# Performance work log

Measured on AMD Instinct MI355X. Metric: run time of the kernel, lower is better.

## Reference

```python
import jax, jax.numpy as jnp
import numpy as np

PAD = 0  # padding_index
BIG = 10000.0

B, S = 1024, 128
V, E, H, T = 200, 512, 512, 24


def setup_inputs() -> dict:
    key = jax.random.key(0)
    ks = jax.random.split(key, 12)
    sequences = jax.random.randint(ks[0], (B, S), 0, V, dtype=jnp.int32)
    labels = jax.random.randint(ks[1], (B, S), 0, T, dtype=jnp.int32)
    true_lengths = jax.random.randint(ks[2], (B,), 1, S, dtype=jnp.int32)
    emb = jax.random.normal(ks[3], (V, E), dtype=jnp.float32) * 0.1
    emb = emb.at[PAD].set(0.0)  # nn.Embedding padding_idx zeros that row
    w1 = jax.random.normal(ks[4], (H, H), dtype=jnp.float32) * (1.0 / np.sqrt(H))
    b1 = jax.random.normal(ks[5], (H,), dtype=jnp.float32) * 0.01
    w2 = jax.random.normal(ks[6], (T, H), dtype=jnp.float32) * (1.0 / np.sqrt(H))
    b2 = jax.random.normal(ks[7], (T,), dtype=jnp.float32) * 0.01
    start_trans = jax.random.uniform(ks[8], (T,), jnp.float32, -0.1, 0.1)
    end_trans = jax.random.uniform(ks[9], (T,), jnp.float32, -0.1, 0.1)
    transitions = jax.random.uniform(ks[10], (T, T), jnp.float32, -0.1, 0.1)
    return {"sequences": sequences, "labels": labels, "true_lengths": true_lengths,
            "emb": emb, "w1": w1, "b1": b1, "w2": w2, "b2": b2,
            "start_trans": start_trans, "end_trans": end_trans, "transitions": transitions}


def _emissions(sequences, emb, w1, b1, w2, b2):
    pad_mask = (sequences == PAD).astype(jnp.float32)  # [B,S]
    x = emb[sequences]                                  # [B,S,E]
    h = jax.nn.relu(x @ w1.T + b1)                      # [B,S,H]
    scores = jax.nn.relu(h @ w2.T + b2)                 # [B,S,T]
    scores = scores.at[:, :, PAD].add(pad_mask * BIG)
    return scores


def _crf_nll_mean(emissions, labels, start_trans, end_trans, transitions):
    # emissions [B,S,T], labels [B,S]; mask = all ones (none passed in forward)
    # numerator: score of gold path
    em_gold = jnp.take_along_axis(emissions, labels[..., None], axis=2)[..., 0]  # [B,S]
    num = (start_trans[labels[:, 0]]
           + em_gold.sum(axis=1)
           + transitions[labels[:, :-1], labels[:, 1:]].sum(axis=1)
           + end_trans[labels[:, -1]])  # [B]
    # denominator: forward algorithm via scan over time
    em_t = jnp.swapaxes(emissions, 0, 1)  # [S,B,T]
    alpha0 = start_trans[None, :] + em_t[0]  # [B,T]

    def step(alpha, emit):
        # alpha [B,T_prev], transitions [T_prev,T_next], emit [B,T_next]
        nxt = jax.nn.logsumexp(alpha[:, :, None] + transitions[None] + emit[:, None, :], axis=1)
        return nxt, None

    alpha, _ = jax.lax.scan(step, alpha0, em_t[1:])
    denom = jax.nn.logsumexp(alpha + end_trans[None, :], axis=1)  # [B]
    llh = num - denom
    return -jnp.mean(llh)


def reference(sequences, labels, true_lengths, emb, w1, b1, w2, b2,
              start_trans, end_trans, transitions):
    emissions = _emissions(sequences, emb, w1, b1, w2, b2)
    return _crf_nll_mean(emissions, labels, start_trans, end_trans, transitions)
```

## Files before the change

### kernel.cpp

```cpp
#include <hip/hip_runtime.h>
#include <math.h>

#define PAD_IDX 0
#define BIGV 10000.0f
constexpr int B_ = 1024, S_ = 128, V_ = 200, E_ = 512, H_ = 512, T_ = 24;

constexpr int OFF_H  = 262144;
constexpr int OFF_EM = 364544;
constexpr int OFF_W  = 369344;
constexpr int OFF_MX = 374144;
constexpr int OFF_GP = 374344;

typedef __attribute__((ext_vector_type(8)))  short    bf8frag;
typedef __attribute__((ext_vector_type(16))) float    facc16;
typedef __attribute__((ext_vector_type(4)))  unsigned u32x4;

__device__ __forceinline__ unsigned short f2bf(float f) {
    unsigned u = __float_as_uint(f);
    u += 0x7fffu + ((u >> 16) & 1u);
    return (unsigned short)(u >> 16);
}
__device__ __forceinline__ unsigned pkbf(float lo, float hi) {
    const unsigned a = __float_as_uint(lo), b = __float_as_uint(hi);
    return ((a + 0x8000u) >> 16) | ((b + 0x8000u) & 0xffff0000u);
}

__global__ __launch_bounds__(256) void transpose_kernel(
    const float* __restrict__ w1, unsigned short* __restrict__ w1Tb,
    float* __restrict__ out)
{
    __shared__ float tile[64][65];
    const int bi = blockIdx.x >> 3, bj = blockIdx.x & 7;
    const int tx = threadIdx.x & 63, r0 = (threadIdx.x >> 6) * 16;
    if (blockIdx.x == 0 && threadIdx.x == 0) out[0] = 0.f;
    #pragma unroll
    for (int m = 0; m < 16; ++m) {
        const int r = r0 + m;
        tile[r][tx] = w1[(size_t)(bi * 64 + r) * 512 + bj * 64 + tx];
    }
    __syncthreads();
    #pragma unroll
    for (int m = 0; m < 16; ++m) {
        const int r = r0 + m;
        w1Tb[(size_t)(bj * 64 + r) * 512 + bi * 64 + tx] = f2bf(tile[tx][r]);
    }
}

__global__ __launch_bounds__(256) void h_kernel(
    const float* __restrict__ emb, const unsigned short* __restrict__ w1Tb,
    const float* __restrict__ b1, float* __restrict__ h_ws)
{
    __shared__ float xi[2 * E_];
    __shared__ float part_s[4][64][8];
    const int pair = blockIdx.x >> 1, half = blockIdx.x & 1;
    const int v0 = pair * 2, v1 = v0 + 1;
    const int tid = threadIdx.x;
    {
        const float* __restrict__ x0 = emb + (size_t)v0 * E_;
        const float* __restrict__ x1 = emb + (size_t)v1 * E_;
        #pragma unroll
        for (int m = 0; m < 2; ++m) {
            const int k = tid + m * 256;
            xi[2 * k]     = x0[k];
            xi[2 * k + 1] = x1[k];
        }
    }
    __syncthreads();
    const int part = tid >> 6, quad = tid & 63;
    const int t0 = half * 256 + quad * 4, k0 = part * 128;
    float a0 = 0.f, a1 = 0.f, a2 = 0.f, a3 = 0.f;
    float c0 = 0.f, c1 = 0.f, c2 = 0.f, c3 = 0.f;
    const unsigned short* __restrict__ wp = w1Tb + (size_t)k0 * H_ + t0;
    const float2* __restrict__ xp = (const float2*)xi + k0;
    #pragma unroll 4
    for (int i = 0; i < 128; ++i) {
        const uint2 wu = *(const uint2*)(wp + (size_t)i * H_);
        const float2 x = xp[i];
        const float w0 = __uint_as_float(wu.x << 16);
        const float w1v = __uint_as_float(wu.x & 0xffff0000u);
        const float w2v = __uint_as_float(wu.y << 16);
        const float w3v = __uint_as_float(wu.y & 0xffff0000u);
        a0 = fmaf(w0,  x.x, a0); a1 = fmaf(w1v, x.x, a1);
        a2 = fmaf(w2v, x.x, a2); a3 = fmaf(w3v, x.x, a3);
        c0 = fmaf(w0,  x.y, c0); c1 = fmaf(w1v, x.y, c1);
        c2 = fmaf(w2v, x.y, c2); c3 = fmaf(w3v, x.y, c3);
    }
    part_s[part][quad][0] = a0; part_s[part][quad][1] = a1;
    part_s[part][quad][2] = a2; part_s[part][quad][3] = a3;
    part_s[part][quad][4] = c0; part_s[part][quad][5] = c1;
    part_s[part][quad][6] = c2; part_s[part][quad][7] = c3;
    __syncthreads();
    {
        const int q2 = tid >> 2, r0 = tid & 3;
        const float s0 = (part_s[0][q2][r0]     + part_s[1][q2][r0])
                       + (part_s[2][q2][r0]     + part_s[3][q2][r0]);
        const float s1 = (part_s[0][q2][r0 + 4] + part_s[1][q2][r0 + 4])
                       + (part_s[2][q2][r0 + 4] + part_s[3][q2][r0 + 4]);
        const int t = half * 256 + tid;
        const float bb = b1[t];
        h_ws[(size_t)v0 * H_ + t] = fmaxf(s0 + bb, 0.f);
        h_ws[(size_t)v1 * H_ + t] = fmaxf(s1 + bb, 0.f);
    }
}

__global__ __launch_bounds__(256) void emis_kernel(
    const float* __restrict__ h_ws, const float* __restrict__ w2,
    const float* __restrict__ b2, float* __restrict__ em_table,
    float* __restrict__ w_table, float* __restrict__ emax_arr)
{
    __shared__ float em_row[32];
    const int v = blockIdx.x;
    const int t = threadIdx.x;
    const int wave = t >> 6, lane = t & 63;
    const float* __restrict__ hrow = h_ws + (size_t)v * H_;
    for (int jj2 = 0; jj2 < 6; ++jj2) {
        const int jo = wave * 6 + jj2;
        float part = 0.f;
        #pragma unroll
        for (int m = 0; m < H_ / 64; ++m) {
            const int k = lane + m * 64;
            part = fmaf(hrow[k], w2[(size_t)jo * H_ + k], part);
        }
        #pragma unroll
        for (int off = 32; off; off >>= 1)
            part += __shfl_xor(part, off, 64);
        if (lane == 0) {
            float val = fmaxf(part + b2[jo], 0.f);
            if (v == 0 && jo == PAD_IDX) val += BIGV;
            em_row[jo] = val;
        }
    }
    __syncthreads();
    if (t < 32) {
        float x = (t < T_) ? em_row[t] : -INFINITY;
        float mx = x;
        #pragma unroll
        for (int off = 16; off; off >>= 1)
            mx = fmaxf(mx, __shfl_xor(mx, off, 32));
        if (t < T_) {
            em_table[v * T_ + t] = x;
            w_table[v * T_ + t]  = __expf(x - mx);
        }
        if (t == 0) emax_arr[v] = mx;
    }
}

__global__ __launch_bounds__(256) void gold_kernel(
    const int* __restrict__ seq, const int* __restrict__ labels,
    const float* __restrict__ start_t, const float* __restrict__ end_t,
    const float* __restrict__ trans, const float* __restrict__ em_table,
    const float* __restrict__ emax_arr, float* __restrict__ gp_ws)
{
    const int grp = threadIdx.x >> 5, j = threadIdx.x & 31;
    const int b = blockIdx.x * 8 + grp;
    const int* __restrict__ srow = seq + (size_t)b * S_;
    const int* __restrict__ lrow = labels + (size_t)b * S_;
    float gp = 0.f;
    #pragma unroll
    for (int r = 0; r < 4; ++r) {
        const int s = j + r * 32;
        const int tk = srow[s], ls = lrow[s];
        gp += em_table[tk * T_ + ls];
        if (s >= 1) gp -= emax_arr[tk];
        if (s < S_ - 1) gp += trans[ls * T_ + lrow[s + 1]];
        if (s == 0) gp += start_t[ls];
        if (s == S_ - 1) gp += end_t[ls];
    }
    #pragma unroll
    for (int off = 16; off; off >>= 1)
        gp += __shfl_xor(gp, off, 32);
    if (j == 0) gp_ws[b] = gp;
}

__global__ __launch_bounds__(128) void crf_kernel(
    const int* __restrict__ seq,
    const float* __restrict__ start_t, const float* __restrict__ end_t,
    const float* __restrict__ trans, const float* __restrict__ em_table,
    const float* __restrict__ w_table, const float* __restrict__ gp_ws,
    float* __restrict__ out)
{
    __shared__ __align__(16) float w_s[V_ * T_];
    __shared__ int   tok_s[S_ * 32];
    __shared__ float meet_s[64 * 12];
    __shared__ float logb_s[64];
    const int tid = threadIdx.x;
    const int g = blockIdx.x;

    for (int i = tid; i < V_ * T_ / 4; i += 128)
        ((float4*)w_s)[i] = ((const float4*)w_table)[i];
    {
        const int bq = tid & 31, c = tid >> 5;
        const int* __restrict__ src = seq + (size_t)(g * 32 + bq) * S_ + c * 32;
        #pragma unroll 4
        for (int i = 0; i < 32; ++i)
            tok_s[(c * 32 + i) * 32 + bq] = src[i];
    }
    __syncthreads();

    const bool isF = (tid < 64);
    const int lane = tid & 63;
    const int n = lane & 31;
    const int h = lane >> 5;

    u32x4 A1p, A2p;
    {
        float a1e[8], a2e[8];
        #pragma unroll
        for (int j = 0; j < 8; ++j) {
            const int k1 = 8 * h + j;
            const int k2 = 16 + 8 * h + j;
            float v1 = 0.f, v2 = 0.f;
            if (n < T_) {
                v1 = __expf(isF ? trans[k1 * T_ + n] : trans[n * T_ + k1]);
                if (k2 < T_)
                    v2 = __expf(isF ? trans[k2 * T_ + n] : trans[n * T_ + k2]);
            }
            a1e[j] = v1; a2e[j] = v2;
        }
        #pragma unroll
        for (int r = 0; r < 4; ++r) {
            A1p[r] = pkbf(a1e[2 * r], a1e[2 * r + 1]);
            A2p[r] = pkbf(a2e[2 * r], a2e[2 * r + 1]);
        }
    }

    float logacc;
    u32x4 B1p, B2p;
    {
        const int tokI = tok_s[(isF ? 0 : (S_ - 1)) * 32 + n];
        float q1[8], q2[8];
        if (isF) {
            float e1[8], e2[8];
            #pragma unroll
            for (int j = 0; j < 8; ++j) { e1[j] = 0.f; e2[j] = 0.f; }
            float mx = -INFINITY;
            #pragma unroll
            for (int j = 0; j < 8; ++j) {
                const int r1 = 8 * h + j;
                e1[j] = start_t[r1] + em_table[tokI * T_ + r1];
                mx = fmaxf(mx, e1[j]);
            }
            if (h == 0) {
                #pragma unroll
                for (int j = 0; j < 8; ++j) {
                    const int r2 = 16 + j;
                    e2[j] = start_t[r2] + em_table[tokI * T_ + r2];
                    mx = fmaxf(mx, e2[j]);
                }
            }
            mx = fmaxf(mx, __shfl_xor(mx, 32, 64));
            #pragma unroll
            for (int j = 0; j < 8; ++j) {
                q1[j] = __expf(e1[j] - mx);
                q2[j] = (h == 0) ? __expf(e2[j] - mx) : 0.f;
            }
            logacc = mx;
        } else {
            #pragma unroll
            for (int j = 0; j < 8; ++j) {
                const int r1 = 8 * h + j;
                q1[j] = w_s[tokI * T_ + r1] * __expf(end_t[r1]);
                const int r2 = 16 + j;
                q2[j] = (h == 0) ? w_s[tokI * T_ + r2] * __expf(end_t[r2]) : 0.f;
            }
            logacc = 0.f;
        }
        #pragma unroll
        for (int r = 0; r < 4; ++r) {
            B1p[r] = pkbf(q1[2 * r], q1[2 * r + 1]);
            B2p[r] = pkbf(q2[2 * r], q2[2 * r + 1]);
        }
    }

    const int dir  = isF ? 1 : -1;
    const int offi = isF ? 1 : (S_ - 2);

    float4 Wc0, Wc1, Wc2;
    {
        const int tk = tok_s[offi * 32 + n];
        const float* wb = w_s + tk * T_ + 4 * h;
        Wc0 = *(const float4*)(wb);
        Wc1 = *(const float4*)(wb + 8);
        Wc2 = *(const float4*)(wb + 16);
    }

    float d[12];
    for (int s = 1; s <= 63; ++s) {
        const int sn = (s < 63) ? (s + 1) : 63;
        const int tkN = tok_s[(offi + dir * (sn - 1)) * 32 + n];
        const float* wbn = w_s + tkN * T_ + 4 * h;
        const float4 Wn0 = *(const float4*)(wbn);
        const float4 Wn1 = *(const float4*)(wbn + 8);
        const float4 Wn2 = *(const float4*)(wbn + 16);

        facc16 acc;
        #pragma unroll
        for (int r = 0; r < 16; ++r) acc[r] = 0.f;
        acc = __builtin_amdgcn_mfma_f32_32x32x16_bf16(
                  __builtin_bit_cast(bf8frag, A2p),
                  __builtin_bit_cast(bf8frag, B2p), acc, 0, 0, 0);
        acc = __builtin_amdgcn_mfma_f32_32x32x16_bf16(
                  __builtin_bit_cast(bf8frag, A1p),
                  __builtin_bit_cast(bf8frag, B1p), acc, 0, 0, 0);

        d[0] = acc[0]*Wc0.x;  d[1] = acc[1]*Wc0.y;  d[2]  = acc[2]*Wc0.z;  d[3]  = acc[3]*Wc0.w;
        d[4] = acc[4]*Wc1.x;  d[5] = acc[5]*Wc1.y;  d[6]  = acc[6]*Wc1.z;  d[7]  = acc[7]*Wc1.w;
        d[8] = acc[8]*Wc2.x;  d[9] = acc[9]*Wc2.y;  d[10] = acc[10]*Wc2.z; d[11] = acc[11]*Wc2.w;

        if ((s & 15) == 0 || s == 63) {
            float mx = d[0];
            #pragma unroll
            for (int r = 1; r < 12; ++r) mx = fmaxf(mx, d[r]);
            mx = fmaxf(mx, __shfl_xor(mx, 32, 64));
            const float inv = 1.0f / mx;
            #pragma unroll
            for (int r = 0; r < 12; ++r) d[r] *= inv;
            logacc += __logf(mx);
        }

        const unsigned P0 = pkbf(d[0], d[1]),  P1 = pkbf(d[2], d[3]);
        const unsigned P2 = pkbf(d[4], d[5]),  P3 = pkbf(d[6], d[7]);
        const unsigned P4 = pkbf(d[8], d[9]),  P5 = pkbf(d[10], d[11]);
        const unsigned XP0 = (unsigned)__shfl_xor((int)P0, 32, 64);
        const unsigned XP1 = (unsigned)__shfl_xor((int)P1, 32, 64);
        const unsigned XP2 = (unsigned)__shfl_xor((int)P2, 32, 64);
        const unsigned XP3 = (unsigned)__shfl_xor((int)P3, 32, 64);
        const unsigned XP4 = (unsigned)__shfl_xor((int)P4, 32, 64);
        const unsigned XP5 = (unsigned)__shfl_xor((int)P5, 32, 64);
        B1p[0] = h ? XP2 : P0;  B1p[1] = h ? XP3 : P1;
        B1p[2] = h ? P2  : XP0; B1p[3] = h ? P3  : XP1;
        B2p[0] = h ? 0u  : P4;  B2p[1] = h ? 0u  : P5;
        B2p[2] = h ? 0u  : XP4; B2p[3] = h ? 0u  : XP5;

        Wc0 = Wn0; Wc1 = Wn1; Wc2 = Wn2;
    }

    if (!isF) {
        #pragma unroll
        for (int r = 0; r < 12; ++r) meet_s[lane * 12 + r] = d[r];
        logb_s[lane] = logacc;
    }
    __syncthreads();
    if (isF) {
        facc16 acc;
        #pragma unroll
        for (int r = 0; r < 16; ++r) acc[r] = 0.f;
        acc = __builtin_amdgcn_mfma_f32_32x32x16_bf16(
                  __builtin_bit_cast(bf8frag, A2p),
                  __builtin_bit_cast(bf8frag, B2p), acc, 0, 0, 0);
        acc = __builtin_amdgcn_mfma_f32_32x32x16_bf16(
                  __builtin_bit_cast(bf8frag, A1p),
                  __builtin_bit_cast(bf8frag, B1p), acc, 0, 0, 0);
        float dot = 0.f;
        #pragma unroll
        for (int r = 0; r < 12; ++r)
            dot = fmaf(acc[r], meet_s[lane * 12 + r], dot);
        dot += __shfl_xor(dot, 32, 64);
        const float denom = logacc + logb_s[lane] + __logf(dot);
        float val = 0.f;
        if (h == 0)
            val = (denom - gp_ws[g * 32 + n]) * (1.0f / (float)B_);
        #pragma unroll
        for (int off = 32; off; off >>= 1)
            val += __shfl_xor(val, off, 64);
        if (lane == 0) atomicAdd(out, val);
    }
}

extern "C" void kernel_launch(void* const* d_in, const int* in_sizes, int n_in,
                              void* d_out, int out_size, void* d_ws, size_t ws_size,
                              hipStream_t stream) {
    const int*   seq     = (const int*)d_in[0];
    const int*   labels  = (const int*)d_in[1];
    const float* emb     = (const float*)d_in[3];
    const float* w1      = (const float*)d_in[4];
    const float* b1      = (const float*)d_in[5];
    const float* w2      = (const float*)d_in[6];
    const float* b2      = (const float*)d_in[7];
    const float* start_t = (const float*)d_in[8];
    const float* end_t   = (const float*)d_in[9];
    const float* trans   = (const float*)d_in[10];

    float* ws       = (float*)d_ws;
    unsigned short* w1Tb = (unsigned short*)d_ws;
    float* h_ws     = ws + OFF_H;
    float* em_table = ws + OFF_EM;
    float* w_table  = ws + OFF_W;
    float* emax_arr = ws + OFF_MX;
    float* gp_ws    = ws + OFF_GP;
    float* out      = (float*)d_out;

    transpose_kernel<<<64, 256, 0, stream>>>(w1, w1Tb, out);
    h_kernel<<<200, 256, 0, stream>>>(emb, w1Tb, b1, h_ws);
    emis_kernel<<<V_, 256, 0, stream>>>(h_ws, w2, b2, em_table, w_table, emax_arr);
    gold_kernel<<<B_ / 8, 256, 0, stream>>>(seq, labels, start_t, end_t, trans,
                                            em_table, emax_arr, gp_ws);
    crf_kernel<<<B_ / 32, 128, 0, stream>>>(seq, start_t, end_t, trans,
                                            em_table, w_table, gp_ws, out);
}
```

Baseline: 119.6 us.

## Fuse gold-path scoring into CRF kernel using extra warps per block

Removes the separate gold_kernel launch and folds gold-path score computation into crf_kernel. Blocks grow from 128 to 256 threads: the first two wavefronts run the forward/backward MFMA recurrence and the two new ones compute gold scores from shared tokens into a shared accumulator. Each step's two MFMAs now write separate accumulators so they no longer depend on each other. This saves a launch and a global round trip for gold scores. In exchange the barrier sits inside divergent branches, which is fragile, and the gold warps finish before the recurrence, so their latency is hidden only if they overlap.

```diff
diff --git a/kernel.cpp b/kernel.cpp
--- a/kernel.cpp
+++ b/kernel.cpp
@@ -9,7 +9,6 @@
 constexpr int OFF_EM = 364544;
 constexpr int OFF_W  = 369344;
 constexpr int OFF_MX = 374144;
-constexpr int OFF_GP = 374344;
 
 typedef __attribute__((ext_vector_type(8)))  short    bf8frag;
 typedef __attribute__((ext_vector_type(16))) float    facc16;
@@ -145,225 +144,230 @@
     }
 }
 
-__global__ __launch_bounds__(256) void gold_kernel(
+__global__ __launch_bounds__(256) void crf_kernel(
     const int* __restrict__ seq, const int* __restrict__ labels,
     const float* __restrict__ start_t, const float* __restrict__ end_t,
     const float* __restrict__ trans, const float* __restrict__ em_table,
-    const float* __restrict__ emax_arr, float* __restrict__ gp_ws)
-{
-    const int grp = threadIdx.x >> 5, j = threadIdx.x & 31;
-    const int b = blockIdx.x * 8 + grp;
-    const int* __restrict__ srow = seq + (size_t)b * S_;
-    const int* __restrict__ lrow = labels + (size_t)b * S_;
-    float gp = 0.f;
-    #pragma unroll
-    for (int r = 0; r < 4; ++r) {
-        const int s = j + r * 32;
-        const int tk = srow[s], ls = lrow[s];
-        gp += em_table[tk * T_ + ls];
-        if (s >= 1) gp -= emax_arr[tk];
-        if (s < S_ - 1) gp += trans[ls * T_ + lrow[s + 1]];
-        if (s == 0) gp += start_t[ls];
-        if (s == S_ - 1) gp += end_t[ls];
-    }
-    #pragma unroll
-    for (int off = 16; off; off >>= 1)
-        gp += __shfl_xor(gp, off, 32);
-    if (j == 0) gp_ws[b] = gp;
-}
-
-__global__ __launch_bounds__(128) void crf_kernel(
-    const int* __restrict__ seq,
-    const float* __restrict__ start_t, const float* __restrict__ end_t,
-    const float* __restrict__ trans, const float* __restrict__ em_table,
-    const float* __restrict__ w_table, const float* __restrict__ gp_ws,
+    const float* __restrict__ w_table, const float* __restrict__ emax_arr,
     float* __restrict__ out)
 {
     __shared__ __align__(16) float w_s[V_ * T_];
     __shared__ int   tok_s[S_ * 32];
     __shared__ float meet_s[64 * 12];
     __shared__ float logb_s[64];
+    __shared__ float gp_s[32];
     const int tid = threadIdx.x;
     const int g = blockIdx.x;
 
-    for (int i = tid; i < V_ * T_ / 4; i += 128)
+    for (int i = tid; i < V_ * T_ / 4; i += 256)
         ((float4*)w_s)[i] = ((const float4*)w_table)[i];
     {
         const int bq = tid & 31, c = tid >> 5;
-        const int* __restrict__ src = seq + (size_t)(g * 32 + bq) * S_ + c * 32;
-        #pragma unroll 4
-        for (int i = 0; i < 32; ++i)
-            tok_s[(c * 32 + i) * 32 + bq] = src[i];
-    }
+        const int* __restrict__ src = seq + (size_t)(g * 32 + bq) * S_ + c * 16;
+        #pragma unroll
+        for (int i = 0; i < 16; ++i)
+            tok_s[(c * 16 + i) * 32 + bq] = src[i];
+    }
+    if (tid < 32) gp_s[tid] = 0.f;
     __syncthreads();
 
-    const bool isF = (tid < 64);
-    const int lane = tid & 63;
-    const int n = lane & 31;
-    const int h = lane >> 5;
-
-    u32x4 A1p, A2p;
-    {
-        float a1e[8], a2e[8];
-        #pragma unroll
-        for (int j = 0; j < 8; ++j) {
-            const int k1 = 8 * h + j;
-            const int k2 = 16 + 8 * h + j;
-            float v1 = 0.f, v2 = 0.f;
-            if (n < T_) {
-                v1 = __expf(isF ? trans[k1 * T_ + n] : trans[n * T_ + k1]);
-                if (k2 < T_)
-                    v2 = __expf(isF ? trans[k2 * T_ + n] : trans[n * T_ + k2]);
+    if (tid < 128) {
+        const bool isF = (tid < 64);
+        const int lane = tid & 63;
+        const int n = lane & 31;
+        const int h = lane >> 5;
+
+        u32x4 A1p, A2p;
+        {
+            float a1e[8], a2e[8];
+            #pragma unroll
+            for (int j = 0; j < 8; ++j) {
+                const int k1 = 8 * h + j;
+                const int k2 = 16 + 8 * h + j;
+                float v1 = 0.f, v2 = 0.f;
+                if (n < T_) {
+                    v1 = __expf(isF ? trans[k1 * T_ + n] : trans[n * T_ + k1]);
+                    if (k2 < T_)
+                        v2 = __expf(isF ? trans[k2 * T_ + n] : trans[n * T_ + k2]);
+                }
+                a1e[j] = v1; a2e[j] = v2;
             }
-            a1e[j] = v1; a2e[j] = v2;
-        }
-        #pragma unroll
-        for (int r = 0; r < 4; ++r) {
-            A1p[r] = pkbf(a1e[2 * r], a1e[2 * r + 1]);
-            A2p[r] = pkbf(a2e[2 * r], a2e[2 * r + 1]);
-        }
-    }
-
-    float logacc;
-    u32x4 B1p, B2p;
-    {
-        const int tokI = tok_s[(isF ? 0 : (S_ - 1)) * 32 + n];
-        float q1[8], q2[8];
+            #pragma unroll
+            for (int r = 0; r < 4; ++r) {
+                A1p[r] = pkbf(a1e[2 * r], a1e[2 * r + 1]);
+                A2p[r] = pkbf(a2e[2 * r], a2e[2 * r + 1]);
+            }
+        }
+
+        float logacc;
+        u32x4 B1p, B2p;
+        {
+            const int tokI = tok_s[(isF ? 0 : (S_ - 1)) * 32 + n];
+            float q1[8], q2[8];
+            if (isF) {
+                float e1[8], e2[8];
+                #pragma unroll
+                for (int j = 0; j < 8; ++j) { e1[j] = 0.f; e2[j] = 0.f; }
+                float mx = -INFINITY;
+                #pragma unroll
+                for (int j = 0; j < 8; ++j) {
+                    const int r1 = 8 * h + j;
+                    e1[j] = start_t[r1] + em_table[tokI * T_ + r1];
+                    mx = fmaxf(mx, e1[j]);
+                }
+                if (h == 0) {
+                    #pragma unroll
+                    for (int j = 0; j < 8; ++j) {
+                        const int r2 = 16 + j;
+                        e2[j] = start_t[r2] + em_table[tokI * T_ + r2];
+                        mx = fmaxf(mx, e2[j]);
+                    }
+                }
+                mx = fmaxf(mx, __shfl_xor(mx, 32, 64));
+                #pragma unroll
+                for (int j = 0; j < 8; ++j) {
+                    q1[j] = __expf(e1[j] - mx);
+                    q2[j] = (h == 0) ? __expf(e2[j] - mx) : 0.f;
+                }
+                logacc = mx;
+            } else {
+                #pragma unroll
+                for (int j = 0; j < 8; ++j) {
+                    const int r1 = 8 * h + j;
+                    q1[j] = w_s[tokI * T_ + r1] * __expf(end_t[r1]);
+                    const int r2 = 16 + j;
+                    q2[j] = (h == 0) ? w_s[tokI * T_ + r2] * __expf(end_t[r2]) : 0.f;
+                }
+                logacc = 0.f;
+            }
+            #pragma unroll
+            for (int r = 0; r < 4; ++r) {
+                B1p[r] = pkbf(q1[2 * r], q1[2 * r + 1]);
+                B2p[r] = pkbf(q2[2 * r], q2[2 * r + 1]);
+            }
+        }
+
+        const int dir  = isF ? 1 : -1;
+        const int offi = isF ? 1 : (S_ - 2);
+
+        float4 Wc0, Wc1, Wc2;
+        {
+            const int tk = tok_s[offi * 32 + n];
+            const float* wb = w_s + tk * T_ + 4 * h;
+            Wc0 = *(const float4*)(wb);
+            Wc1 = *(const float4*)(wb + 8);
+            Wc2 = *(const float4*)(wb + 16);
+        }
+
+        float d[12];
+        for (int s = 1; s <= 63; ++s) {
+            const int sn = (s < 63) ? (s + 1) : 63;
+            const int tkN = tok_s[(offi + dir * (sn - 1)) * 32 + n];
+            const float* wbn = w_s + tkN * T_ + 4 * h;
+            const float4 Wn0 = *(const float4*)(wbn);
+            const float4 Wn1 = *(const float4*)(wbn + 8);
+            const float4 Wn2 = *(const float4*)(wbn + 16);
+
+            facc16 accA, accB;
+            #pragma unroll
+            for (int r = 0; r < 16; ++r) { accA[r] = 0.f; accB[r] = 0.f; }
+            accA = __builtin_amdgcn_mfma_f32_32x32x16_bf16(
+                       __builtin_bit_cast(bf8frag, A1p),
+                       __builtin_bit_cast(bf8frag, B1p), accA, 0, 0, 0);
+            accB = __builtin_amdgcn_mfma_f32_32x32x16_bf16(
+                       __builtin_bit_cast(bf8frag, A2p),
+                       __builtin_bit_cast(bf8frag, B2p), accB, 0, 0, 0);
+
+            d[0]  = (accA[0]  + accB[0] ) * Wc0.x;
+            d[1]  = (accA[1]  + accB[1] ) * Wc0.y;
+            d[2]  = (accA[2]  + accB[2] ) * Wc0.z;
+            d[3]  = (accA[3]  + accB[3] ) * Wc0.w;
+            d[4]  = (accA[4]  + accB[4] ) * Wc1.x;
+            d[5]  = (accA[5]  + accB[5] ) * Wc1.y;
+            d[6]  = (accA[6]  + accB[6] ) * Wc1.z;
+            d[7]  = (accA[7]  + accB[7] ) * Wc1.w;
+            d[8]  = (accA[8]  + accB[8] ) * Wc2.x;
+            d[9]  = (accA[9]  + accB[9] ) * Wc2.y;
+            d[10] = (accA[10] + accB[10]) * Wc2.z;
+            d[11] = (accA[11] + accB[11]) * Wc2.w;
+
+            if ((s & 15) == 0 || s == 63) {
+                float mx = d[0];
+                #pragma unroll
+                for (int r = 1; r < 12; ++r) mx = fmaxf(mx, d[r]);
+                mx = fmaxf(mx, __shfl_xor(mx, 32, 64));
+                const float inv = 1.0f / mx;
+                #pragma unroll
+                for (int r = 0; r < 12; ++r) d[r] *= inv;
+                logacc += __logf(mx);
+            }
+
+            const unsigned P0 = pkbf(d[0], d[1]),  P1 = pkbf(d[2], d[3]);
+            const unsigned P2 = pkbf(d[4], d[5]),  P3 = pkbf(d[6], d[7]);
+            const unsigned P4 = pkbf(d[8], d[9]),  P5 = pkbf(d[10], d[11]);
+            const unsigned XP0 = (unsigned)__shfl_xor((int)P0, 32, 64);
+            const unsigned XP1 = (unsigned)__shfl_xor((int)P1, 32, 64);
+            const unsigned XP2 = (unsigned)__shfl_xor((int)P2, 32, 64);
+            const unsigned XP3 = (unsigned)__shfl_xor((int)P3, 32, 64);
+            const unsigned XP4 = (unsigned)__shfl_xor((int)P4, 32, 64);
+            const unsigned XP5 = (unsigned)__shfl_xor((int)P5, 32, 64);
+            B1p[0] = h ? XP2 : P0;  B1p[1] = h ? XP3 : P1;
+            B1p[2] = h ? P2  : XP0; B1p[3] = h ? P3  : XP1;
+            B2p[0] = h ? 0u  : P4;  B2p[1] = h ? 0u  : P5;
+            B2p[2] = h ? 0u  : XP4; B2p[3] = h ? 0u  : XP5;
+
+            Wc0 = Wn0; Wc1 = Wn1; Wc2 = Wn2;
+        }
+
+        if (!isF) {
+            #pragma unroll
+            for (int r = 0; r < 12; ++r) meet_s[lane * 12 + r] = d[r];
+            logb_s[lane] = logacc;
+        }
+        __syncthreads();
         if (isF) {
-            float e1[8], e2[8];
-            #pragma unroll
-            for (int j = 0; j < 8; ++j) { e1[j] = 0.f; e2[j] = 0.f; }
-            float mx = -INFINITY;
-            #pragma unroll
-            for (int j = 0; j < 8; ++j) {
-                const int r1 = 8 * h + j;
-                e1[j] = start_t[r1] + em_table[tokI * T_ + r1];
-                mx = fmaxf(mx, e1[j]);
-            }
-            if (h == 0) {
-                #pragma unroll
-                for (int j = 0; j < 8; ++j) {
-                    const int r2 = 16 + j;
-                    e2[j] = start_t[r2] + em_table[tokI * T_ + r2];
-                    mx = fmaxf(mx, e2[j]);
-                }
-            }
-            mx = fmaxf(mx, __shfl_xor(mx, 32, 64));
-            #pragma unroll
-            for (int j = 0; j < 8; ++j) {
-                q1[j] = __expf(e1[j] - mx);
-                q2[j] = (h == 0) ? __expf(e2[j] - mx) : 0.f;
-            }
-            logacc = mx;
-        } else {
-            #pragma unroll
-            for (int j = 0; j < 8; ++j) {
-                const int r1 = 8 * h + j;
-                q1[j] = w_s[tokI * T_ + r1] * __expf(end_t[r1]);
-                const int r2 = 16 + j;
-                q2[j] = (h == 0) ? w_s[tokI * T_ + r2] * __expf(end_t[r2]) : 0.f;
-            }
-            logacc = 0.f;
-        }
-        #pragma unroll
-        for (int r = 0; r < 4; ++r) {
-            B1p[r] = pkbf(q1[2 * r], q1[2 * r + 1]);
-            B2p[r] = pkbf(q2[2 * r], q2[2 * r + 1]);
-        }
-    }
-
-    const int dir  = isF ? 1 : -1;
-    const int offi = isF ? 1 : (S_ - 2);
-
-    float4 Wc0, Wc1, Wc2;
-    {
-        const int tk = tok_s[offi * 32 + n];
-        const float* wb = w_s + tk * T_ + 4 * h;
-        Wc0 = *(const float4*)(wb);
-        Wc1 = *(const float4*)(wb + 8);
-        Wc2 = *(const float4*)(wb + 16);
-    }
-
-    float d[12];
-    for (int s = 1; s <= 63; ++s) {
-        const int sn = (s < 63) ? (s + 1) : 63;
-        const int tkN = tok_s[(offi + dir * (sn - 1)) * 32 + n];
-        const float* wbn = w_s + tkN * T_ + 4 * h;
-        const float4 Wn0 = *(const float4*)(wbn);
-        const float4 Wn1 = *(const float4*)(wbn + 8);
-        const float4 Wn2 = *(const float4*)(wbn + 16);
-
-        facc16 acc;
-        #pragma unroll
-        for (int r = 0; r < 16; ++r) acc[r] = 0.f;
-        acc = __builtin_amdgcn_mfma_f32_32x32x16_bf16(
-                  __builtin_bit_cast(bf8frag, A2p),
-                  __builtin_bit_cast(bf8frag, B2p), acc, 0, 0, 0);
-        acc = __builtin_amdgcn_mfma_f32_32x32x16_bf16(
-                  __builtin_bit_cast(bf8frag, A1p),
-                  __builtin_bit_cast(bf8frag, B1p), acc, 0, 0, 0);
-
-        d[0] = acc[0]*Wc0.x;  d[1] = acc[1]*Wc0.y;  d[2]  = acc[2]*Wc0.z;  d[3]  = acc[3]*Wc0.w;
-        d[4] = acc[4]*Wc1.x;  d[5] = acc[5]*Wc1.y;  d[6]  = acc[6]*Wc1.z;  d[7]  = acc[7]*Wc1.w;
-        d[8] = acc[8]*Wc2.x;  d[9] = acc[9]*Wc2.y;  d[10] = acc[10]*Wc2.z; d[11] = acc[11]*Wc2.w;
-
-        if ((s & 15) == 0 || s == 63) {
-            float mx = d[0];
-            #pragma unroll
-            for (int r = 1; r < 12; ++r) mx = fmaxf(mx, d[r]);
-            mx = fmaxf(mx, __shfl_xor(mx, 32, 64));
-            const float inv = 1.0f / mx;
-            #pragma unroll
-            for (int r = 0; r < 12; ++r) d[r] *= inv;
-            logacc += __logf(mx);
-        }
-
-        const unsigned P0 = pkbf(d[0], d[1]),  P1 = pkbf(d[2], d[3]);
-        const unsigned P2 = pkbf(d[4], d[5]),  P3 = pkbf(d[6], d[7]);
-        const unsigned P4 = pkbf(d[8], d[9]),  P5 = pkbf(d[10], d[11]);
-        const unsigned XP0 = (unsigned)__shfl_xor((int)P0, 32, 64);
-        const unsigned XP1 = (unsigned)__shfl_xor((int)P1, 32, 64);
-        const unsigned XP2 = (unsigned)__shfl_xor((int)P2, 32, 64);
-        const unsigned XP3 = (unsigned)__shfl_xor((int)P3, 32, 64);
-        const unsigned XP4 = (unsigned)__shfl_xor((int)P4, 32, 64);
-        const unsigned XP5 = (unsigned)__shfl_xor((int)P5, 32, 64);
-        B1p[0] = h ? XP2 : P0;  B1p[1] = h ? XP3 : P1;
-        B1p[2] = h ? P2  : XP0; B1p[3] = h ? P3  : XP1;
-        B2p[0] = h ? 0u  : P4;  B2p[1] = h ? 0u  : P5;
-        B2p[2] = h ? 0u  : XP4; B2p[3] = h ? 0u  : XP5;
-
-        Wc0 = Wn0; Wc1 = Wn1; Wc2 = Wn2;
-    }
-
-    if (!isF) {
-        #pragma unroll
-        for (int r = 0; r < 12; ++r) meet_s[lane * 12 + r] = d[r];
-        logb_s[lane] = logacc;
-    }
-    __syncthreads();
-    if (isF) {
-        facc16 acc;
-        #pragma unroll
-        for (int r = 0; r < 16; ++r) acc[r] = 0.f;
-        acc = __builtin_amdgcn_mfma_f32_32x32x16_bf16(
-                  __builtin_bit_cast(bf8frag, A2p),
-                  __builtin_bit_cast(bf8frag, B2p), acc, 0, 0, 0);
-        acc = __builtin_amdgcn_mfma_f32_32x32x16_bf16(
-                  __builtin_bit_cast(bf8frag, A1p),
-                  __builtin_bit_cast(bf8frag, B1p), acc, 0, 0, 0);
-        float dot = 0.f;
-        #pragma unroll
-        for (int r = 0; r < 12; ++r)
-            dot = fmaf(acc[r], meet_s[lane * 12 + r], dot);
-        dot += __shfl_xor(dot, 32, 64);
-        const float denom = logacc + logb_s[lane] + __logf(dot);
-        float val = 0.f;
-        if (h == 0)
-            val = (denom - gp_ws[g * 32 + n]) * (1.0f / (float)B_);
-        #pragma unroll
-        for (int off = 32; off; off >>= 1)
-            val += __shfl_xor(val, off, 64);
-        if (lane == 0) atomicAdd(out, val);
+            facc16 accA, accB;
+            #pragma unroll
+            for (int r = 0; r < 16; ++r) { accA[r] = 0.f; accB[r] = 0.f; }
+            accA = __builtin_amdgcn_mfma_f32_32x32x16_bf16(
+                       __builtin_bit_cast(bf8frag, A1p),
+                       __builtin_bit_cast(bf8frag, B1p), accA, 0, 0, 0);
+            accB = __builtin_amdgcn_mfma_f32_32x32x16_bf16(
+                       __builtin_bit_cast(bf8frag, A2p),
+                       __builtin_bit_cast(bf8frag, B2p), accB, 0, 0, 0);
+            float dot = 0.f;
+            #pragma unroll
+            for (int r = 0; r < 12; ++r)
+                dot = fmaf(accA[r] + accB[r], meet_s[lane * 12 + r], dot);
+            dot += __shfl_xor(dot, 32, 64);
+            const float denom = logacc + logb_s[lane] + __logf(dot);
+            float val = 0.f;
+            if (h == 0)
+                val = (denom - gp_s[n]) * (1.0f / (float)B_);
+            #pragma unroll
+            for (int off = 32; off; off >>= 1)
+                val += __shfl_xor(val, off, 64);
+            if (lane == 0) atomicAdd(out, val);
+        }
+    } else {
+        const int t2 = tid - 128;
+        const int n = t2 & 31;
+        const int r = t2 >> 5;
+        const int b = g * 32 + n;
+        const int* __restrict__ lrow = labels + (size_t)b * S_;
+        float gp = 0.f;
+        for (int i = 0; i < 32; ++i) {
+            const int s = r * 32 + i;
+            const int tk = tok_s[s * 32 + n];
+            const int ls = lrow[s];
+            gp += em_table[tk * T_ + ls];
+            if (s >= 1) gp -= emax_arr[tk];
+            if (s < S_ - 1) gp += trans[ls * T_ + lrow[s + 1]];
+            if (s == 0) gp += start_t[ls];
+            if (s == S_ - 1) gp += end_t[ls];
+        }
+        atomicAdd(&gp_s[n], gp);
+        __syncthreads();
     }
 }
 
@@ -381,20 +385,17 @@
     const float* end_t   = (const float*)d_in[9];
     const float* trans   = (const float*)d_in[10];
 
-    float* ws       = (float*)d_ws;
+    float* ws            = (float*)d_ws;
     unsigned short* w1Tb = (unsigned short*)d_ws;
-    float* h_ws     = ws + OFF_H;
-    float* em_table = ws + OFF_EM;
-    float* w_table  = ws + OFF_W;
-    float* emax_arr = ws + OFF_MX;
-    float* gp_ws    = ws + OFF_GP;
-    float* out      = (float*)d_out;
+    float* h_ws          = ws + OFF_H;
+    float* em_table      = ws + OFF_EM;
+    float* w_table       = ws + OFF_W;
+    float* emax_arr      = ws + OFF_MX;
+    float* out           = (float*)d_out;
 
     transpose_kernel<<<64, 256, 0, stream>>>(w1, w1Tb, out);
     h_kernel<<<200, 256, 0, stream>>>(emb, w1Tb, b1, h_ws);
     emis_kernel<<<V_, 256, 0, stream>>>(h_ws, w2, b2, em_table, w_table, emax_arr);
-    gold_kernel<<<B_ / 8, 256, 0, stream>>>(seq, labels, start_t, end_t, trans,
-                                            em_table, emax_arr, gp_ws);
-    crf_kernel<<<B_ / 32, 128, 0, stream>>>(seq, start_t, end_t, trans,
-                                            em_table, w_table, gp_ws, out);
-}
+    crf_kernel<<<B_ / 32, 256, 0, stream>>>(seq, labels, start_t, end_t, trans,
+                                            em_table, w_table, emax_arr, out);
+}
```

After: 117.6 us. About the same (-1.7%).
